# Optimization experiments

Hardware: AMD Instinct MI355X
Metric: run time of the kernel (lower is better)

Reference implementation:

```python
import jax, jax.numpy as jnp
import numpy as np
from functools import partial

D = 1024
H = 4 * D
E = 8
K_TOP = 2
B, T = 4, 2048
NEG_INF = jnp.float32(-1e30)


def setup_inputs() -> dict:
    key = jax.random.key(0)
    ks = jax.random.split(key, 12)
    s = 0.02
    return {
        "x": jax.random.normal(ks[0], (B, T, D), jnp.float32),
        "noise": jax.random.normal(ks[1], (B, T, E), jnp.float32),
        "gate_w": jax.random.normal(ks[2], (E, D), jnp.float32) * s,
        "gate_b": jnp.zeros((E,), jnp.float32),
        "var_w": jax.random.normal(ks[3], (E, D), jnp.float32) * s,
        "var_b": jnp.zeros((E,), jnp.float32),
        "w1": jax.random.normal(ks[4], (E, H, D), jnp.float32) * s,
        "b1": jnp.zeros((E, H), jnp.float32),
        "w2": jax.random.normal(ks[5], (E, D, H), jnp.float32) * s,
        "b2": jnp.zeros((E, D), jnp.float32),
    }


def reference(x, noise, gate_w, gate_b, var_w, var_b, w1, b1, w2, b2):
    # Noisy top-k gating
    logits = jnp.einsum("btd,ed->bte", x, gate_w) + gate_b          # [B,T,E]
    std = jax.nn.softplus(jnp.einsum("btd,ed->bte", x, var_w) + var_b)
    noisy = logits + noise * std                                      # [B,T,E]
    _, idx = jax.lax.top_k(noisy, K_TOP)                              # [B,T,K]
    # boolean top-k mask over experts
    mask = (idx[..., None] == jnp.arange(E)).any(axis=-2)             # [B,T,E]
    coef = jax.nn.softmax(jnp.where(mask, noisy, NEG_INF), axis=-1)   # zeros outside top-k

    # Combine: sum_e coef_e * FFN_e(x). coef is exactly 0 for non-selected
    # experts, so this equals the masked gather/scatter math. Scan over the
    # small expert dim to avoid a [E,B,T,H] intermediate.
    coef_e = jnp.moveaxis(coef, -1, 0)                                # [E,B,T]

    def body(acc, ew):
        w1e, b1e, w2e, b2e, ce = ew
        h = jax.nn.relu(jnp.einsum("btd,hd->bth", x, w1e) + b1e)
        y = jnp.einsum("bth,dh->btd", h, w2e) + b2e
        return acc + y * ce[..., None], None

    out, _ = jax.lax.scan(body, jnp.zeros_like(x), (w1, b1, w2, b2, coef_e))
    return out
```

## Files before the change

kernel.cpp:

```cpp
#include <hip/hip_runtime.h>
#include <hip/hip_bf16.h>
#include <math.h>

#define NTOK 8192
#define DD   1024
#define HH   4096
#define NE   8
#define BM 128
#define BN 128
#define BK 64
#define SLOT_CAP (2 * NTOK + NE * BM)

typedef __bf16 bf16;
typedef __bf16 bf16x8 __attribute__((ext_vector_type(8)));
typedef __bf16 bf16x4 __attribute__((ext_vector_type(4)));
typedef float  f32x4  __attribute__((ext_vector_type(4)));

typedef __attribute__((address_space(3))) unsigned char lds_u8;
typedef const __attribute__((address_space(1))) unsigned char g_u8;

__device__ __forceinline__ void gload16(const bf16* g, bf16* l) {
  __builtin_amdgcn_global_load_lds((g_u8*)g, (lds_u8*)l, 16, 0, 0);
}

__device__ __forceinline__ float softplus_f(float v) {
  return fmaxf(v, 0.f) + log1pf(expf(-fabsf(v)));
}

__global__ __launch_bounds__(64) void moe_gate_kernel(
    const float* __restrict__ x, const float* __restrict__ noise,
    const float* __restrict__ gate_w, const float* __restrict__ gate_b,
    const float* __restrict__ var_w,  const float* __restrict__ var_b,
    float* __restrict__ coef2, int* __restrict__ t2e, int* __restrict__ counts,
    bf16* __restrict__ xb)
{
  const int t = blockIdx.x;
  const int lane = threadIdx.x;
  const float* xt = x + (size_t)t * DD;
  bf16* xbt = xb + (size_t)t * DD;
  float pg[NE], pv[NE];
  #pragma unroll
  for (int e = 0; e < NE; ++e) { pg[e] = 0.f; pv[e] = 0.f; }
  #pragma unroll 4
  for (int i = 0; i < DD / 64; ++i) {
    const int d = lane + i * 64;
    const float xv = xt[d];
    xbt[d] = (bf16)xv;
    #pragma unroll
    for (int e = 0; e < NE; ++e) {
      pg[e] = fmaf(xv, gate_w[e * DD + d], pg[e]);
      pv[e] = fmaf(xv, var_w[e * DD + d], pv[e]);
    }
  }
  #pragma unroll
  for (int e = 0; e < NE; ++e) {
    #pragma unroll
    for (int off = 32; off; off >>= 1) {
      pg[e] += __shfl_xor(pg[e], off);
      pv[e] += __shfl_xor(pv[e], off);
    }
  }
  if (lane == 0) {
    float noisy[NE];
    #pragma unroll
    for (int e = 0; e < NE; ++e) {
      const float lg = pg[e] + gate_b[e];
      const float sd = softplus_f(pv[e] + var_b[e]);
      noisy[e] = lg + noise[t * NE + e] * sd;
    }
    int i1 = 0; float n1 = noisy[0];
    #pragma unroll
    for (int e = 1; e < NE; ++e) if (noisy[e] > n1) { n1 = noisy[e]; i1 = e; }
    int i2 = -1; float n2 = -3.0e38f;
    #pragma unroll
    for (int e = 0; e < NE; ++e) if (e != i1 && noisy[e] > n2) { n2 = noisy[e]; i2 = e; }
    const float e2 = expf(n2 - n1);
    const float den = 1.f + e2;
    coef2[t * 2 + 0] = 1.f / den;
    coef2[t * 2 + 1] = e2 / den;
    t2e[t * 2 + 0] = i1;
    t2e[t * 2 + 1] = i2;
    atomicAdd(&counts[i1], 1);
    atomicAdd(&counts[i2], 1);
  }
}

__global__ void moe_offsets_kernel(const int* __restrict__ counts, int* __restrict__ po) {
  if (threadIdx.x == 0) {
    int acc = 0;
    po[0] = 0;
    for (int e = 0; e < NE; ++e) {
      acc += ((counts[e] + BM - 1) / BM) * BM;
      po[e + 1] = acc;
    }
  }
}

__global__ __launch_bounds__(256) void moe_scatter_kernel(
    const int* __restrict__ t2e, const float* __restrict__ coef2,
    const int* __restrict__ po, int* __restrict__ cnt2,
    int* __restrict__ assign_tok, float* __restrict__ slot_coef)
{
  const int t = blockIdx.x * 256 + threadIdx.x;
  if (t >= NTOK) return;
  #pragma unroll
  for (int k = 0; k < 2; ++k) {
    const int e = t2e[t * 2 + k];
    const int pos = atomicAdd(&cnt2[e], 1);
    const int slot = po[e] + pos;
    assign_tok[slot] = t;
    slot_coef[slot] = coef2[t * 2 + k];
  }
}

__global__ __launch_bounds__(256) void cvt2_bf16_kernel(
    const float* __restrict__ s1, bf16* __restrict__ d1, int n41,
    const float* __restrict__ s2, bf16* __restrict__ d2, int n42)
{
  for (int i = blockIdx.x * 256 + threadIdx.x; i < n41 + n42; i += gridDim.x * 256) {
    const float* s = (i < n41) ? s1 : s2;
    bf16* d = (i < n41) ? d1 : d2;
    const int j = (i < n41) ? i : i - n41;
    const float4 f = ((const float4*)s)[j];
    bf16x4 v;
    v[0] = (bf16)f.x; v[1] = (bf16)f.y; v[2] = (bf16)f.z; v[3] = (bf16)f.w;
    ((bf16x4*)d)[j] = v;
  }
}

template<int KDIM, int NCOLS, int SY, bool FFN1>
__global__ __launch_bounds__(256) void moe_gemm_kernel(
    const bf16* __restrict__ Asrc, const bf16* __restrict__ Wsrc,
    const float* __restrict__ bias,
    const int* __restrict__ assign_tok, const float* __restrict__ slot_coef,
    const int* __restrict__ po,
    bf16* __restrict__ hout, float* __restrict__ out,
    int chunk_base, int gx)
{
  __shared__ bf16 As[BM][BK];
  __shared__ bf16 Bs[BN][BK];
  __shared__ int toks[BM];

  const int nwg = gridDim.x;
  const int lin = blockIdx.x;
  const int q = nwg >> 3, r = nwg & 7;
  const int xcd = lin & 7, idx = lin >> 3;
  const int wg = (xcd < r ? xcd * (q + 1) : r * (q + 1) + (xcd - r) * q) + idx;

  const int ss = gx * SY;
  const int stripe = wg / ss;
  const int rem = wg - stripe * ss;
  const int bx = rem / SY;
  const int by = stripe * SY + (rem - bx * SY);

  const int po8 = po[NE];
  const int row0 = chunk_base + bx * BM;
  if (row0 >= po8) return;
  int e = 0;
  while (row0 >= po[e + 1]) ++e;
  const int bn0 = by * BN;
  const bf16* We = Wsrc + (size_t)e * ((size_t)HH * DD);
  const int tid = threadIdx.x, lane = tid & 63, wave = tid >> 6;
  if (tid < BM) toks[tid] = assign_tok[row0 + tid];
  __syncthreads();

  const int rin = lane >> 3;
  const int c8s = ((lane & 7) ^ rin) * 8;
  const bf16* asrc[4];
  const bf16* bsrc[4];
  #pragma unroll
  for (int i = 0; i < 4; ++i) {
    const int c = wave * 4 + i;
    const int row = c * 8 + rin;
    int ar;
    if constexpr (FFN1) {
      const int s = toks[row];
      ar = s < 0 ? 0 : s;
    } else {
      ar = row0 - chunk_base + row;
    }
    asrc[i] = Asrc + (size_t)ar * KDIM + c8s;
    bsrc[i] = We + (size_t)(bn0 + row) * KDIM + c8s;
  }

  const int la = lane & 15, hi = lane >> 4;
  const int wm = (wave >> 1) * 64, wn = (wave & 1) * 64;
  f32x4 acc[4][4];
  #pragma unroll
  for (int m = 0; m < 4; ++m)
    #pragma unroll
    for (int n = 0; n < 4; ++n) acc[m][n] = {0.f, 0.f, 0.f, 0.f};

  for (int k0 = 0; k0 < KDIM; k0 += BK) {
    #pragma unroll
    for (int i = 0; i < 4; ++i) gload16(asrc[i] + k0, &As[(wave * 4 + i) * 8][0]);
    #pragma unroll
    for (int i = 0; i < 4; ++i) gload16(bsrc[i] + k0, &Bs[(wave * 4 + i) * 8][0]);
    __syncthreads();
    #pragma unroll
    for (int ks = 0; ks < 2; ++ks) {
      bf16x8 af[4], bff[4];
      #pragma unroll
      for (int m = 0; m < 4; ++m) {
        const int row = wm + m * 16 + la;
        const int c8 = (ks * 4 + hi) ^ (row & 7);
        af[m] = *(const bf16x8*)(&As[row][c8 * 8]);
      }
      #pragma unroll
      for (int n = 0; n < 4; ++n) {
        const int row = wn + n * 16 + la;
        const int c8 = (ks * 4 + hi) ^ (row & 7);
        bff[n] = *(const bf16x8*)(&Bs[row][c8 * 8]);
      }
      #pragma unroll
      for (int m = 0; m < 4; ++m)
        #pragma unroll
        for (int n = 0; n < 4; ++n)
          acc[m][n] = __builtin_amdgcn_mfma_f32_16x16x32_bf16(af[m], bff[n], acc[m][n], 0, 0, 0);
    }
    __syncthreads();
  }

  if constexpr (FFN1) {
    const int hrow0 = row0 - chunk_base;
    #pragma unroll
    for (int n = 0; n < 4; ++n) {
      const int col = bn0 + wn + n * 16 + la;
      const float bb = bias[e * NCOLS + col];
      #pragma unroll
      for (int m = 0; m < 4; ++m) {
        const int rbase = wm + m * 16 + hi * 4;
        #pragma unroll
        for (int rr = 0; rr < 4; ++rr) {
          float v = acc[m][n][rr] + bb;
          v = v > 0.f ? v : 0.f;
          hout[(size_t)(hrow0 + rbase + rr) * HH + col] = (bf16)v;
        }
      }
    }
  } else {
    #pragma unroll
    for (int n = 0; n < 4; ++n) {
      const int col = bn0 + wn + n * 16 + la;
      const float bb = bias[e * NCOLS + col];
      #pragma unroll
      for (int m = 0; m < 4; ++m) {
        const int rbase = wm + m * 16 + hi * 4;
        #pragma unroll
        for (int rr = 0; rr < 4; ++rr) {
          const int trow = rbase + rr;
          const int tok = toks[trow];
          if (tok >= 0) {
            const float c = slot_coef[row0 + trow];
            atomicAdd(out + (size_t)tok * DD + col, c * (acc[m][n][rr] + bb));
          }
        }
      }
    }
  }
}

extern "C" void kernel_launch(void* const* d_in, const int* in_sizes, int n_in,
                              void* d_out, int out_size, void* d_ws, size_t ws_size,
                              hipStream_t stream) {
  const float* x      = (const float*)d_in[0];
  const float* noise  = (const float*)d_in[1];
  const float* gate_w = (const float*)d_in[2];
  const float* gate_b = (const float*)d_in[3];
  const float* var_w  = (const float*)d_in[4];
  const float* var_b  = (const float*)d_in[5];
  const float* w1     = (const float*)d_in[6];
  const float* b1     = (const float*)d_in[7];
  const float* w2     = (const float*)d_in[8];
  const float* b2     = (const float*)d_in[9];
  float* out = (float*)d_out;
  (void)in_sizes; (void)n_in; (void)out_size;

  char* ws = (char*)d_ws;
  size_t off = 0;
  auto alloc = [&](size_t bytes) {
    off = (off + 255) & ~(size_t)255;
    size_t o = off;
    off += bytes;
    return o;
  };
  bf16*  xb         = (bf16*)(ws + alloc((size_t)NTOK * DD * 2));
  float* coef2      = (float*)(ws + alloc((size_t)NTOK * 2 * 4));
  int*   t2e        = (int*)(ws + alloc((size_t)NTOK * 2 * 4));
  int*   counts     = (int*)(ws + alloc(64));
  int*   cnt2       = counts + 8;
  int*   po         = (int*)(ws + alloc(64));
  int*   assign_tok = (int*)(ws + alloc((size_t)SLOT_CAP * 4));
  float* slot_coef  = (float*)(ws + alloc((size_t)SLOT_CAP * 4));
  bf16*  w1b        = (bf16*)(ws + alloc((size_t)NE * HH * DD * 2));
  bf16*  w2b        = (bf16*)(ws + alloc((size_t)NE * DD * HH * 2));
  off = (off + 255) & ~(size_t)255;
  const size_t h_avail = ws_size > off ? ws_size - off : 0;
  int chunk_rows = (int)(h_avail / ((size_t)HH * 2));
  chunk_rows = (chunk_rows / BM) * BM;
  if (chunk_rows < BM) chunk_rows = BM;
  if (chunk_rows > SLOT_CAP) chunk_rows = SLOT_CAP;
  bf16* hbuf = (bf16*)(ws + off);

  hipMemsetAsync(counts, 0, 64, stream);
  hipMemsetAsync(assign_tok, 0xFF, (size_t)SLOT_CAP * 4, stream);
  hipMemsetAsync(out, 0, (size_t)NTOK * DD * 4, stream);

  moe_gate_kernel<<<NTOK, 64, 0, stream>>>(x, noise, gate_w, gate_b, var_w, var_b,
                                           coef2, t2e, counts, xb);
  moe_offsets_kernel<<<1, 64, 0, stream>>>(counts, po);
  moe_scatter_kernel<<<NTOK / 256, 256, 0, stream>>>(t2e, coef2, po, cnt2,
                                                     assign_tok, slot_coef);
  cvt2_bf16_kernel<<<2048, 256, 0, stream>>>(w1, w1b, NE * HH * DD / 4,
                                             w2, w2b, NE * DD * HH / 4);

  const int rounds = (SLOT_CAP + chunk_rows - 1) / chunk_rows;
  for (int r = 0; r < rounds; ++r) {
    const int cb = r * chunk_rows;
    const int rows_here = (cb + chunk_rows <= SLOT_CAP) ? chunk_rows : (SLOT_CAP - cb);
    const int gx = rows_here / BM;
    moe_gemm_kernel<DD, HH, 8, true><<<gx * (HH / BN), 256, 0, stream>>>(
        xb, w1b, b1, assign_tok, slot_coef, po, hbuf, nullptr, cb, gx);
    moe_gemm_kernel<HH, DD, 4, false><<<gx * (DD / BN), 256, 0, stream>>>(
        hbuf, w2b, b2, assign_tok, slot_coef, po, nullptr, out, cb, gx);
  }
}
```

Measured before the change: 943.2 us.

## Widen GEMM N-tile to 256, split-K FFN2, simplify tile mapping, batch gate tokens

The expert GEMM tile grows from 128x128 to 128x256, so each wave holds a 4x8 accumulator grid and every A-tile load from LDS feeds twice as many MFMAs. The second GEMM splits its K dimension in two across blockIdx.z, with the bias added only by the first split, to get more workgroups now that there are fewer N tiles. The stripe-based tile mapping is replaced by plain row-major and column-major orders. The gate kernel processes 16 tokens per block and uses float4 loads. The costs are more accumulator registers per thread, which may lower occupancy, and twice as many atomic adds into the output from the split-K GEMM.

```diff
diff --git a/kernel.cpp b/kernel.cpp
--- a/kernel.cpp
+++ b/kernel.cpp
@@ -7,7 +7,7 @@
 #define HH   4096
 #define NE   8
 #define BM 128
-#define BN 128
+#define BN 256
 #define BK 64
 #define SLOT_CAP (2 * NTOK + NE * BM)
 
@@ -34,54 +34,62 @@
     float* __restrict__ coef2, int* __restrict__ t2e, int* __restrict__ counts,
     bf16* __restrict__ xb)
 {
-  const int t = blockIdx.x;
   const int lane = threadIdx.x;
-  const float* xt = x + (size_t)t * DD;
-  bf16* xbt = xb + (size_t)t * DD;
-  float pg[NE], pv[NE];
-  #pragma unroll
-  for (int e = 0; e < NE; ++e) { pg[e] = 0.f; pv[e] = 0.f; }
-  #pragma unroll 4
-  for (int i = 0; i < DD / 64; ++i) {
-    const int d = lane + i * 64;
-    const float xv = xt[d];
-    xbt[d] = (bf16)xv;
+  const float4* gw4 = (const float4*)gate_w;
+  const float4* vw4 = (const float4*)var_w;
+  for (int tt = 0; tt < 16; ++tt) {
+    const int t = blockIdx.x * 16 + tt;
+    const float4* x4 = (const float4*)(x + (size_t)t * DD);
+    bf16x4* xb4 = (bf16x4*)(xb + (size_t)t * DD);
+    float pg[NE], pv[NE];
+    #pragma unroll
+    for (int e = 0; e < NE; ++e) { pg[e] = 0.f; pv[e] = 0.f; }
+    #pragma unroll
+    for (int i = 0; i < DD / 256; ++i) {
+      const int d4 = i * 64 + lane;
+      const float4 f = x4[d4];
+      bf16x4 v;
+      v[0] = (bf16)f.x; v[1] = (bf16)f.y; v[2] = (bf16)f.z; v[3] = (bf16)f.w;
+      xb4[d4] = v;
+      #pragma unroll
+      for (int e = 0; e < NE; ++e) {
+        const float4 g = gw4[e * 256 + d4];
+        pg[e] = fmaf(f.x, g.x, fmaf(f.y, g.y, fmaf(f.z, g.z, fmaf(f.w, g.w, pg[e]))));
+        const float4 w = vw4[e * 256 + d4];
+        pv[e] = fmaf(f.x, w.x, fmaf(f.y, w.y, fmaf(f.z, w.z, fmaf(f.w, w.w, pv[e]))));
+      }
+    }
     #pragma unroll
     for (int e = 0; e < NE; ++e) {
-      pg[e] = fmaf(xv, gate_w[e * DD + d], pg[e]);
-      pv[e] = fmaf(xv, var_w[e * DD + d], pv[e]);
-    }
-  }
-  #pragma unroll
-  for (int e = 0; e < NE; ++e) {
-    #pragma unroll
-    for (int off = 32; off; off >>= 1) {
-      pg[e] += __shfl_xor(pg[e], off);
-      pv[e] += __shfl_xor(pv[e], off);
-    }
-  }
-  if (lane == 0) {
-    float noisy[NE];
-    #pragma unroll
-    for (int e = 0; e < NE; ++e) {
-      const float lg = pg[e] + gate_b[e];
-      const float sd = softplus_f(pv[e] + var_b[e]);
-      noisy[e] = lg + noise[t * NE + e] * sd;
-    }
-    int i1 = 0; float n1 = noisy[0];
-    #pragma unroll
-    for (int e = 1; e < NE; ++e) if (noisy[e] > n1) { n1 = noisy[e]; i1 = e; }
-    int i2 = -1; float n2 = -3.0e38f;
-    #pragma unroll
-    for (int e = 0; e < NE; ++e) if (e != i1 && noisy[e] > n2) { n2 = noisy[e]; i2 = e; }
-    const float e2 = expf(n2 - n1);
-    const float den = 1.f + e2;
-    coef2[t * 2 + 0] = 1.f / den;
-    coef2[t * 2 + 1] = e2 / den;
-    t2e[t * 2 + 0] = i1;
-    t2e[t * 2 + 1] = i2;
-    atomicAdd(&counts[i1], 1);
-    atomicAdd(&counts[i2], 1);
+      #pragma unroll
+      for (int off = 32; off; off >>= 1) {
+        pg[e] += __shfl_xor(pg[e], off);
+        pv[e] += __shfl_xor(pv[e], off);
+      }
+    }
+    if (lane == 0) {
+      float noisy[NE];
+      #pragma unroll
+      for (int e = 0; e < NE; ++e) {
+        const float lg = pg[e] + gate_b[e];
+        const float sd = softplus_f(pv[e] + var_b[e]);
+        noisy[e] = lg + noise[t * NE + e] * sd;
+      }
+      int i1 = 0; float n1 = noisy[0];
+      #pragma unroll
+      for (int e = 1; e < NE; ++e) if (noisy[e] > n1) { n1 = noisy[e]; i1 = e; }
+      int i2 = -1; float n2 = -3.0e38f;
+      #pragma unroll
+      for (int e = 0; e < NE; ++e) if (e != i1 && noisy[e] > n2) { n2 = noisy[e]; i2 = e; }
+      const float e2 = expf(n2 - n1);
+      const float den = 1.f + e2;
+      coef2[t * 2 + 0] = 1.f / den;
+      coef2[t * 2 + 1] = e2 / den;
+      t2e[t * 2 + 0] = i1;
+      t2e[t * 2 + 1] = i2;
+      atomicAdd(&counts[i1], 1);
+      atomicAdd(&counts[i2], 1);
+    }
   }
 }
 
@@ -128,7 +136,7 @@
   }
 }
 
-template<int KDIM, int NCOLS, int SY, bool FFN1>
+template<int KDIM, int KSTRIDE, int NCOLS, bool FFN1>
 __global__ __launch_bounds__(256) void moe_gemm_kernel(
     const bf16* __restrict__ Asrc, const bf16* __restrict__ Wsrc,
     const float* __restrict__ bias,
@@ -146,12 +154,9 @@
   const int q = nwg >> 3, r = nwg & 7;
   const int xcd = lin & 7, idx = lin >> 3;
   const int wg = (xcd < r ? xcd * (q + 1) : r * (q + 1) + (xcd - r) * q) + idx;
-
-  const int ss = gx * SY;
-  const int stripe = wg / ss;
-  const int rem = wg - stripe * ss;
-  const int bx = rem / SY;
-  const int by = stripe * SY + (rem - bx * SY);
+  int bx, by;
+  if constexpr (FFN1) { bx = wg % gx; by = wg / gx; }
+  else               { by = wg % (NCOLS / BN); bx = wg / (NCOLS / BN); }
 
   const int po8 = po[NE];
   const int row0 = chunk_base + bx * BM;
@@ -159,7 +164,9 @@
   int e = 0;
   while (row0 >= po[e + 1]) ++e;
   const int bn0 = by * BN;
-  const bf16* We = Wsrc + (size_t)e * ((size_t)HH * DD);
+  const size_t kbase = (size_t)blockIdx.z * KDIM;
+  const bf16* We = Wsrc + (size_t)e * ((size_t)HH * DD) + kbase;
+  const bf16* Asb = Asrc + kbase;
   const int tid = threadIdx.x, lane = tid & 63, wave = tid >> 6;
   if (tid < BM) toks[tid] = assign_tok[row0 + tid];
   __syncthreads();
@@ -167,11 +174,10 @@
   const int rin = lane >> 3;
   const int c8s = ((lane & 7) ^ rin) * 8;
   const bf16* asrc[4];
-  const bf16* bsrc[4];
+  const bf16* bsrc[8];
   #pragma unroll
   for (int i = 0; i < 4; ++i) {
-    const int c = wave * 4 + i;
-    const int row = c * 8 + rin;
+    const int row = (wave * 4 + i) * 8 + rin;
     int ar;
     if constexpr (FFN1) {
       const int s = toks[row];
@@ -179,27 +185,31 @@
     } else {
       ar = row0 - chunk_base + row;
     }
-    asrc[i] = Asrc + (size_t)ar * KDIM + c8s;
-    bsrc[i] = We + (size_t)(bn0 + row) * KDIM + c8s;
+    asrc[i] = Asb + (size_t)ar * KSTRIDE + c8s;
+  }
+  #pragma unroll
+  for (int i = 0; i < 8; ++i) {
+    const int row = (wave * 8 + i) * 8 + rin;
+    bsrc[i] = We + (size_t)(bn0 + row) * KSTRIDE + c8s;
   }
 
   const int la = lane & 15, hi = lane >> 4;
-  const int wm = (wave >> 1) * 64, wn = (wave & 1) * 64;
-  f32x4 acc[4][4];
+  const int wm = (wave >> 1) * 64, wn = (wave & 1) * 128;
+  f32x4 acc[4][8];
   #pragma unroll
   for (int m = 0; m < 4; ++m)
     #pragma unroll
-    for (int n = 0; n < 4; ++n) acc[m][n] = {0.f, 0.f, 0.f, 0.f};
+    for (int n = 0; n < 8; ++n) acc[m][n] = {0.f, 0.f, 0.f, 0.f};
 
   for (int k0 = 0; k0 < KDIM; k0 += BK) {
     #pragma unroll
     for (int i = 0; i < 4; ++i) gload16(asrc[i] + k0, &As[(wave * 4 + i) * 8][0]);
     #pragma unroll
-    for (int i = 0; i < 4; ++i) gload16(bsrc[i] + k0, &Bs[(wave * 4 + i) * 8][0]);
+    for (int i = 0; i < 8; ++i) gload16(bsrc[i] + k0, &Bs[(wave * 8 + i) * 8][0]);
     __syncthreads();
     #pragma unroll
     for (int ks = 0; ks < 2; ++ks) {
-      bf16x8 af[4], bff[4];
+      bf16x8 af[4], bff[8];
       #pragma unroll
       for (int m = 0; m < 4; ++m) {
         const int row = wm + m * 16 + la;
@@ -207,7 +217,7 @@
         af[m] = *(const bf16x8*)(&As[row][c8 * 8]);
       }
       #pragma unroll
-      for (int n = 0; n < 4; ++n) {
+      for (int n = 0; n < 8; ++n) {
         const int row = wn + n * 16 + la;
         const int c8 = (ks * 4 + hi) ^ (row & 7);
         bff[n] = *(const bf16x8*)(&Bs[row][c8 * 8]);
@@ -215,7 +225,7 @@
       #pragma unroll
       for (int m = 0; m < 4; ++m)
         #pragma unroll
-        for (int n = 0; n < 4; ++n)
+        for (int n = 0; n < 8; ++n)
           acc[m][n] = __builtin_amdgcn_mfma_f32_16x16x32_bf16(af[m], bff[n], acc[m][n], 0, 0, 0);
     }
     __syncthreads();
@@ -224,7 +234,7 @@
   if constexpr (FFN1) {
     const int hrow0 = row0 - chunk_base;
     #pragma unroll
-    for (int n = 0; n < 4; ++n) {
+    for (int n = 0; n < 8; ++n) {
       const int col = bn0 + wn + n * 16 + la;
       const float bb = bias[e * NCOLS + col];
       #pragma unroll
@@ -239,10 +249,11 @@
       }
     }
   } else {
-    #pragma unroll
-    for (int n = 0; n < 4; ++n) {
+    const bool addb = (blockIdx.z == 0);
+    #pragma unroll
+    for (int n = 0; n < 8; ++n) {
       const int col = bn0 + wn + n * 16 + la;
-      const float bb = bias[e * NCOLS + col];
+      const float bb = addb ? bias[e * NCOLS + col] : 0.f;
       #pragma unroll
       for (int m = 0; m < 4; ++m) {
         const int rbase = wm + m * 16 + hi * 4;
@@ -306,8 +317,8 @@
   hipMemsetAsync(assign_tok, 0xFF, (size_t)SLOT_CAP * 4, stream);
   hipMemsetAsync(out, 0, (size_t)NTOK * DD * 4, stream);
 
-  moe_gate_kernel<<<NTOK, 64, 0, stream>>>(x, noise, gate_w, gate_b, var_w, var_b,
-                                           coef2, t2e, counts, xb);
+  moe_gate_kernel<<<NTOK / 16, 64, 0, stream>>>(x, noise, gate_w, gate_b, var_w, var_b,
+                                                coef2, t2e, counts, xb);
   moe_offsets_kernel<<<1, 64, 0, stream>>>(counts, po);
   moe_scatter_kernel<<<NTOK / 256, 256, 0, stream>>>(t2e, coef2, po, cnt2,
                                                      assign_tok, slot_coef);
@@ -319,9 +330,11 @@
     const int cb = r * chunk_rows;
     const int rows_here = (cb + chunk_rows <= SLOT_CAP) ? chunk_rows : (SLOT_CAP - cb);
     const int gx = rows_here / BM;
-    moe_gemm_kernel<DD, HH, 8, true><<<gx * (HH / BN), 256, 0, stream>>>(
+    dim3 g1(gx * (HH / BN), 1, 1);
+    moe_gemm_kernel<DD, DD, HH, true><<<g1, 256, 0, stream>>>(
         xb, w1b, b1, assign_tok, slot_coef, po, hbuf, nullptr, cb, gx);
-    moe_gemm_kernel<HH, DD, 4, false><<<gx * (DD / BN), 256, 0, stream>>>(
+    dim3 g2(gx * (DD / BN), 1, 2);
+    moe_gemm_kernel<HH / 2, HH, DD, false><<<g2, 256, 0, stream>>>(
         hbuf, w2b, b2, assign_tok, slot_coef, po, nullptr, out, cb, gx);
   }
 }
```

After: 1.254 ms. +32.9%, slower.
